# Performance work log

Hardware: AMD Instinct MI355X
Metric: run time of the kernel (lower is better)

## Reference

```python
import jax, jax.numpy as jnp
import numpy as np
import math

BS, S, D, H, DFF, L = 32, 512, 512, 8, 2048, 2
DK = D // H
K_INDEX = 5
NEG = -1e32


def _xavier(key, shape):
    fan_out, fan_in = shape[-2], shape[-1]
    lim = math.sqrt(6.0 / (fan_in + fan_out))
    return jax.random.uniform(key, shape, minval=-lim, maxval=lim, dtype=jnp.float32)


def _cosine_pe():
    pos = np.arange(S, dtype=np.float32)[:, None]
    div = np.exp(np.arange(0, D, 2, dtype=np.float32) * -(math.log(10000.0) / D))
    pe = np.zeros((S, D), dtype=np.float32)
    pe[:, 0::2] = np.sin(pos * div)
    pe[:, 1::2] = np.cos(pos * div)
    return jnp.asarray(pe)[None]  # [1,S,D]


def setup_inputs() -> dict:
    key = jax.random.key(0)
    ks = jax.random.split(key, 8)
    return {
        'q_embed_data': jax.random.normal(ks[0], (BS, S, D), jnp.float32),
        'qa_embed_data': jax.random.normal(ks[1], (BS, S, D), jnp.float32),
        'pe': _cosine_pe(),
        'Wk': _xavier(ks[2], (L, D, D)), 'bk': jnp.zeros((L, D)),
        'Wv': _xavier(ks[3], (L, D, D)), 'bv': jnp.zeros((L, D)),
        'Wo': _xavier(ks[4], (L, D, D)), 'bo': jnp.zeros((L, D)),
        'W1': _xavier(ks[5], (L, DFF, D)), 'b1': jnp.zeros((L, DFF)),
        'W2': _xavier(ks[6], (L, D, DFF)), 'b2': jnp.zeros((L, D)),
        'ln1w': jnp.ones((L, D)), 'ln1b': jnp.zeros((L, D)),
        'ln2w': jnp.ones((L, D)), 'ln2b': jnp.zeros((L, D)),
    }


def _ln(x, w, b):
    m = jnp.mean(x, axis=-1, keepdims=True)
    v = jnp.mean((x - m) ** 2, axis=-1, keepdims=True)
    return (x - m) / jnp.sqrt(v + 1e-5) * w + b


def _forward(q_embed_data, qa_embed_data, pe, Wk, bk, Wv, bv, Wo, bo,
             W1, b1, W2, b2, ln1w, ln1b, ln2w, ln2b):
    x = q_embed_data + pe[:, :S]
    y = qa_embed_data + pe[:, :S]
    # src_mask = (triu(ones, k=0) == 0): only strictly-lower positions allowed (row 0 fully masked)
    causal = jnp.tril(jnp.ones((S, S), bool), k=-1)
    attn_weights = None
    for l in range(L):
        # kq_same: q uses k_linear
        q = (x @ Wk[l].T + bk[l]).reshape(BS, S, H, DK).transpose(0, 2, 1, 3)
        k = q  # identical projection of identical input (key=query=x)
        v = (y @ Wv[l].T + bv[l]).reshape(BS, S, H, DK).transpose(0, 2, 1, 3)
        scores = jnp.einsum('bhqd,bhkd->bhqk', q, k) / math.sqrt(DK)
        scores = jnp.where(causal, scores, NEG)
        scores = jax.nn.softmax(scores, axis=-1)
        # sparseattn: for rows >= K_INDEX keep only entries >= k-th largest, re-softmax
        sb = scores[:, :, K_INDEX:, :]
        thr = jax.lax.top_k(sb, K_INDEX)[0][..., -1:]  # k-th largest per row
        sb = jnp.where(sb - thr >= 0, sb, NEG)
        scores = jnp.concatenate([scores[:, :, :K_INDEX, :], sb], axis=2)
        scores = jax.nn.softmax(scores, axis=-1)
        attn_weights = scores  # before_dropout_scores (before zero_pad)
        scores = scores.at[:, :, 0, :].set(0.0)  # zero_pad row 0
        out = jnp.einsum('bhqk,bhkd->bhqd', scores, v)
        out = out.transpose(0, 2, 1, 3).reshape(BS, S, D) @ Wo[l].T + bo[l]
        x = _ln(x + out, ln1w[l], ln1b[l])
        ff = jax.nn.relu(x @ W1[l].T + b1[l]) @ W2[l].T + b2[l]
        x = _ln(x + ff, ln2w[l], ln2b[l])
    return x, attn_weights


def reference(q_embed_data, qa_embed_data, pe, Wk, bk, Wv, bv, Wo, bo,
              W1, b1, W2, b2, ln1w, ln1b, ln2w, ln2b):
    return _forward(q_embed_data, qa_embed_data, pe, Wk, bk, Wv, bv, Wo, bo,
                    W1, b1, W2, b2, ln1w, ln1b, ln2w, ln2b)
```

## Files before the change

### kernel.cpp

```cpp
#include <hip/hip_runtime.h>
#include <hip/hip_bf16.h>
#include <math.h>

#define BSZ 32
#define SEQ 512
#define DIM 512
#define NH 8
#define DKH 64
#define DFFN 2048
#define NL 2
#define KIDX 5
#define NEGV -1e32f

typedef float f32x4 __attribute__((ext_vector_type(4)));
typedef short bf16x8 __attribute__((ext_vector_type(8)));
typedef unsigned short ushort_t;
typedef __attribute__((address_space(1))) void gvoid;
typedef __attribute__((address_space(3))) void lvoid;

__device__ __forceinline__ void gload_lds16(const void* g, void* l) {
    __builtin_amdgcn_global_load_lds((gvoid*)(uintptr_t)g, (lvoid*)l, 16, 0, 0);
}

__device__ __forceinline__ float wmaxf(float v) {
    #pragma unroll
    for (int m = 32; m > 0; m >>= 1) v = fmaxf(v, __shfl_xor(v, m));
    return v;
}
__device__ __forceinline__ float wsumf(float v) {
    #pragma unroll
    for (int m = 32; m > 0; m >>= 1) v += __shfl_xor(v, m);
    return v;
}
__device__ __forceinline__ int wsumi(int v) {
    #pragma unroll
    for (int m = 32; m > 0; m >>= 1) v += __shfl_xor(v, m);
    return v;
}

__device__ __forceinline__ unsigned int bf16_rne(float x) {
    unsigned int u = __float_as_uint(x);
    return (u + 0x7fffu + ((u >> 16) & 1u)) >> 16;
}
__device__ __forceinline__ void split3_8(const float* xs, unsigned int* hh,
                                         unsigned int* hm, unsigned int* hl) {
    #pragma unroll
    for (int e = 0; e < 8; e++) {
        float x = xs[e];
        unsigned int h0 = bf16_rne(x);
        float r1 = x - __uint_as_float(h0 << 16);
        unsigned int h1 = bf16_rne(r1);
        float r2 = r1 - __uint_as_float(h1 << 16);
        hh[e] = h0; hm[e] = h1; hl[e] = bf16_rne(r2);
    }
}
__device__ __forceinline__ uint4 pack8(const unsigned int* h) {
    return make_uint4(h[0] | (h[1] << 16), h[2] | (h[3] << 16),
                      h[4] | (h[5] << 16), h[6] | (h[7] << 16));
}

__device__ __forceinline__ f32x4 mfma_bf16(bf16x8 a, bf16x8 b, f32x4 c) {
    return __builtin_amdgcn_mfma_f32_16x16x32_bf16(a, b, c, 0, 0, 0);
}

__global__ void add_pe_old(const float4* __restrict__ q, const float4* __restrict__ qa,
                           const float4* __restrict__ pe, float4* __restrict__ x,
                           float4* __restrict__ y, int n4) {
    int i = blockIdx.x * 256 + threadIdx.x;
    if (i >= n4) return;
    int pi = i & (SEQ * DIM / 4 - 1);
    float4 p = pe[pi];
    float4 a = q[i], b = qa[i];
    x[i] = make_float4(a.x + p.x, a.y + p.y, a.z + p.z, a.w + p.w);
    y[i] = make_float4(b.x + p.x, b.y + p.y, b.z + p.z, b.w + p.w);
}

__global__ void add_pe_new(const float* __restrict__ q, const float* __restrict__ qa,
                           const float* __restrict__ pe, float* __restrict__ x,
                           ushort_t* __restrict__ ypl, size_t yelems, int n8) {
    int i = blockIdx.x * 256 + threadIdx.x;
    if (i >= n8) return;
    size_t base = (size_t)i * 8;
    size_t pb = base & (size_t)(SEQ * DIM - 1);
    float4 a0 = *(const float4*)(q + base), a1 = *(const float4*)(q + base + 4);
    float4 b0 = *(const float4*)(qa + base), b1 = *(const float4*)(qa + base + 4);
    float4 p0 = *(const float4*)(pe + pb), p1 = *(const float4*)(pe + pb + 4);
    float4 x0 = make_float4(a0.x + p0.x, a0.y + p0.y, a0.z + p0.z, a0.w + p0.w);
    float4 x1 = make_float4(a1.x + p1.x, a1.y + p1.y, a1.z + p1.z, a1.w + p1.w);
    *(float4*)(x + base) = x0;
    *(float4*)(x + base + 4) = x1;
    float ys[8] = {b0.x + p0.x, b0.y + p0.y, b0.z + p0.z, b0.w + p0.w,
                   b1.x + p1.x, b1.y + p1.y, b1.z + p1.z, b1.w + p1.w};
    unsigned int hh[8], hm[8], hl[8];
    split3_8(ys, hh, hm, hl);
    *(uint4*)(ypl + base) = pack8(hh);
    *(uint4*)(ypl + yelems + base) = pack8(hm);
    *(uint4*)(ypl + 2 * yelems + base) = pack8(hl);
}

__global__ void split3w(const float* __restrict__ W, ushort_t* __restrict__ out,
                        size_t elems, int n8) {
    int i = blockIdx.x * 256 + threadIdx.x;
    if (i >= n8) return;
    size_t base = (size_t)i * 8;
    float4 a0 = *(const float4*)(W + base), a1 = *(const float4*)(W + base + 4);
    float xs[8] = {a0.x, a0.y, a0.z, a0.w, a1.x, a1.y, a1.z, a1.w};
    unsigned int hh[8], hm[8], hl[8];
    split3_8(xs, hh, hm, hl);
    *(uint4*)(out + base) = pack8(hh);
    *(uint4*)(out + elems + base) = pack8(hm);
    *(uint4*)(out + 2 * elems + base) = pack8(hl);
}

template <int RELU>
__global__ __launch_bounds__(256)
void gemm_bt(const float* __restrict__ A, const float* __restrict__ B,
             const float* __restrict__ bias, float* __restrict__ C,
             int M, int N, int K) {
    __shared__ float As[16][132];
    __shared__ float Bs[16][132];
    const int tid = threadIdx.x;
    const int tx = tid & 15, ty = tid >> 4;
    const int m0 = blockIdx.y * 128, n0 = blockIdx.x * 128;
    float acc[8][8] = {};
    for (int k0 = 0; k0 < K; k0 += 16) {
        #pragma unroll
        for (int s = tid; s < 512; s += 256) {
            int r = s >> 2, c4 = s & 3;
            float4 va = *(const float4*)(A + (size_t)(m0 + r) * K + k0 + c4 * 4);
            As[c4 * 4 + 0][r] = va.x; As[c4 * 4 + 1][r] = va.y;
            As[c4 * 4 + 2][r] = va.z; As[c4 * 4 + 3][r] = va.w;
            float4 vb = *(const float4*)(B + (size_t)(n0 + r) * K + k0 + c4 * 4);
            Bs[c4 * 4 + 0][r] = vb.x; Bs[c4 * 4 + 1][r] = vb.y;
            Bs[c4 * 4 + 2][r] = vb.z; Bs[c4 * 4 + 3][r] = vb.w;
        }
        __syncthreads();
        #pragma unroll
        for (int kk = 0; kk < 16; kk++) {
            float a[8], b[8];
            *(float4*)&a[0] = *(const float4*)&As[kk][ty * 8];
            *(float4*)&a[4] = *(const float4*)&As[kk][ty * 8 + 4];
            *(float4*)&b[0] = *(const float4*)&Bs[kk][tx * 8];
            *(float4*)&b[4] = *(const float4*)&Bs[kk][tx * 8 + 4];
            #pragma unroll
            for (int i = 0; i < 8; i++)
                #pragma unroll
                for (int j = 0; j < 8; j++)
                    acc[i][j] = fmaf(a[i], b[j], acc[i][j]);
        }
        __syncthreads();
    }
    float bv[8];
    *(float4*)&bv[0] = *(const float4*)(bias + n0 + tx * 8);
    *(float4*)&bv[4] = *(const float4*)(bias + n0 + tx * 8 + 4);
    #pragma unroll
    for (int i = 0; i < 8; i++) {
        float out[8];
        #pragma unroll
        for (int j = 0; j < 8; j++) {
            float v = acc[i][j] + bv[j];
            if (RELU) v = fmaxf(v, 0.f);
            out[j] = v;
        }
        float* cp = C + (size_t)(m0 + ty * 8 + i) * N + n0 + tx * 8;
        *(float4*)cp = *(float4*)&out[0];
        *(float4*)(cp + 4) = *(float4*)&out[4];
    }
}

__global__ __launch_bounds__(256)
void scores128_kernel(const float* __restrict__ q, float* __restrict__ pbuf) {
    const int bh = blockIdx.y, b = bh >> 3, h = bh & 7;
    const int x = blockIdx.x;
    const int it = (x >= 6) ? 3 : (x >= 3) ? 2 : (x >= 1) ? 1 : 0;
    const int jt = x - it * (it + 1) / 2;
    const int m0 = it * 128, n0 = jt * 128;
    __shared__ float Qi[64][132];
    __shared__ float Qj[64][132];
    const float* qbase = q + (size_t)b * SEQ * DIM + h * DKH;
    const int tid = threadIdx.x;
    for (int s = tid; s < 2048; s += 256) {
        int row = (s & 15) | ((s >> 8) << 4);
        int c4 = (s >> 4) & 15;
        float4 vi = *(const float4*)(qbase + (size_t)(m0 + row) * DIM + c4 * 4);
        Qi[c4 * 4 + 0][row] = vi.x; Qi[c4 * 4 + 1][row] = vi.y;
        Qi[c4 * 4 + 2][row] = vi.z; Qi[c4 * 4 + 3][row] = vi.w;
        float4 vj = *(const float4*)(qbase + (size_t)(n0 + row) * DIM + c4 * 4);
        Qj[c4 * 4 + 0][row] = vj.x; Qj[c4 * 4 + 1][row] = vj.y;
        Qj[c4 * 4 + 2][row] = vj.z; Qj[c4 * 4 + 3][row] = vj.w;
    }
    __syncthreads();
    const int tx = tid & 15, ty = tid >> 4;
    float acc[8][8] = {};
    #pragma unroll 4
    for (int d = 0; d < 64; d++) {
        float a[8], bb[8];
        *(float4*)&a[0] = *(const float4*)&Qi[d][ty * 8];
        *(float4*)&a[4] = *(const float4*)&Qi[d][ty * 8 + 4];
        *(float4*)&bb[0] = *(const float4*)&Qj[d][tx * 8];
        *(float4*)&bb[4] = *(const float4*)&Qj[d][tx * 8 + 4];
        #pragma unroll
        for (int i = 0; i < 8; i++)
            #pragma unroll
            for (int j = 0; j < 8; j++)
                acc[i][j] = fmaf(a[i], bb[j], acc[i][j]);
    }
    float* prow = pbuf + ((size_t)bh * SEQ + m0) * SEQ + n0;
    #pragma unroll
    for (int i = 0; i < 8; i++) {
        int gi = m0 + ty * 8 + i;
        #pragma unroll
        for (int jq = 0; jq < 2; jq++) {
            float o[4];
            #pragma unroll
            for (int j = 0; j < 4; j++) {
                int gj = n0 + tx * 8 + jq * 4 + j;
                o[j] = (gj < gi) ? acc[i][jq * 4 + j] * 0.125f : NEGV;
            }
            *(float4*)(prow + (size_t)(ty * 8 + i) * SEQ + tx * 8 + jq * 4) = *(float4*)o;
        }
    }
}

template <int RELU, int OUTP, int NP>
__global__ __launch_bounds__(256) void gemm3p(
    const ushort_t* __restrict__ Apl, size_t Aelems, int lda,
    const ushort_t* __restrict__ Bpl, size_t Belems, int ldb,
    const float* __restrict__ bias,
    float* __restrict__ C, ushort_t* __restrict__ Cpl, size_t Celems,
    int ldc, int K) {
    constexpr int BB = NP * 512;
    __shared__ uint4 lds[2 * NP * 512];
    const int tid = threadIdx.x, lane = tid & 63, wid = tid >> 6;
    const int wm = wid >> 1, wn = wid & 1;
    const int m0 = blockIdx.y * 128, n0 = blockIdx.x * 128;
    const int lrow = lane & 15, lkof = (lane >> 4) * 8;
    f32x4 acc[4][4] = {};
    for (int k0 = 0; k0 < K; k0 += 32) {
        #pragma unroll
        for (int t = 0; t < 4 * NP; t++) {
            int cc = wid + t * 4;
            bool isB = cc >= 8 * NP;
            int c2 = isB ? (cc - 8 * NP) : cc;
            int p = c2 >> 3, fi = c2 & 7;
            const ushort_t* pb = isB ? (Bpl + (size_t)p * Belems) : (Apl + (size_t)p * Aelems);
            int ld = isB ? ldb : lda;
            int r0 = isB ? n0 : m0;
            const ushort_t* src = pb + (size_t)(r0 + fi * 16 + lrow) * ld + k0 + lkof;
            gload_lds16(src, &lds[(isB ? BB : 0) + p * 512 + fi * 64]);
        }
        __syncthreads();
        const bf16x8* ldsb = (const bf16x8*)lds;
        bf16x8 afr[4][NP];
        #pragma unroll
        for (int fm = 0; fm < 4; fm++)
            #pragma unroll
            for (int p = 0; p < NP; p++)
                afr[fm][p] = ldsb[p * 512 + (wm * 4 + fm) * 64 + lane];
        #pragma unroll
        for (int fn = 0; fn < 4; fn++) {
            bf16x8 b0 = ldsb[BB + 0 * 512 + (wn * 4 + fn) * 64 + lane];
            bf16x8 b1 = ldsb[BB + 1 * 512 + (wn * 4 + fn) * 64 + lane];
            bf16x8 b2;
            if constexpr (NP == 3) b2 = ldsb[BB + 2 * 512 + (wn * 4 + fn) * 64 + lane];
            #pragma unroll
            for (int fm = 0; fm < 4; fm++) {
                f32x4 t = acc[fm][fn];
                if constexpr (NP == 3) {
                    t = mfma_bf16(afr[fm][0], b0, t);
                    t = mfma_bf16(afr[fm][1], b0, t);
                    t = mfma_bf16(afr[fm][2], b0, t);
                    t = mfma_bf16(afr[fm][0], b1, t);
                    t = mfma_bf16(afr[fm][1], b1, t);
                    t = mfma_bf16(afr[fm][0], b2, t);
                } else {
                    t = mfma_bf16(afr[fm][0], b0, t);
                    t = mfma_bf16(afr[fm][1], b0, t);
                    t = mfma_bf16(afr[fm][0], b1, t);
                }
                acc[fm][fn] = t;
            }
        }
        __syncthreads();
    }
    #pragma unroll
    for (int fm = 0; fm < 4; fm++) {
        int row0 = m0 + (wm * 4 + fm) * 16 + (lane >> 4) * 4;
        #pragma unroll
        for (int fn = 0; fn < 4; fn++) {
            int col = n0 + (wn * 4 + fn) * 16 + (lane & 15);
            float bv = bias[col];
            f32x4 a = acc[fm][fn];
            #pragma unroll
            for (int r = 0; r < 4; r++) {
                int row = row0 + r;
                float val = a[r] + bv;
                if (RELU) val = fmaxf(val, 0.f);
                if constexpr (OUTP == 0) {
                    C[(size_t)row * ldc + col] = val;
                } else {
                    unsigned int h0 = bf16_rne(val);
                    float r1 = val - __uint_as_float(h0 << 16);
                    unsigned int h1 = bf16_rne(r1);
                    size_t o = (size_t)row * ldc + col;
                    Cpl[o] = (ushort_t)h0;
                    Cpl[Celems + o] = (ushort_t)h1;
                    if constexpr (NP == 3) {
                        float r2 = r1 - __uint_as_float(h1 << 16);
                        Cpl[2 * Celems + o] = (ushort_t)bf16_rne(r2);
                    }
                }
            }
        }
    }
}

template <int MODE, int TN>
__global__ __launch_bounds__(256) void mm6(const float* __restrict__ Aall,
                                           const float* __restrict__ Ball,
                                           float* __restrict__ Call,
                                           const float* __restrict__ bias,
                                           int lda, int ldb, int ldc, int K) {
    constexpr int BFR = TN / 16;
    constexpr int MFR = (TN == 128) ? 4 : 2;
    constexpr int BBASE = 3 * 8 * 64;
    __shared__ uint4 lds[3 * 8 * 64 + 3 * BFR * 64];

    const int tid = threadIdx.x, lane = tid & 63, wid = tid >> 6;
    const int wm = (TN == 128) ? (wid >> 1) : wid;
    const int wn = (TN == 128) ? (wid & 1) : 0;

    const float* A;
    const float* B;
    float* C;
    int m0, n0, kmax;
    if constexpr (MODE <= 1) {
        m0 = blockIdx.y * 128;
        n0 = blockIdx.x * 128;
        A = Aall; B = Ball; C = Call;
        kmax = K;
    } else {
        const int bh = blockIdx.y, b = bh >> 3, h = bh & 7, rb = blockIdx.x;
        m0 = rb * 128; n0 = 0;
        A = Aall + (size_t)bh * SEQ * SEQ;
        B = Ball + (size_t)bh * DKH * SEQ;
        C = Call + ((size_t)b * SEQ) * DIM + h * DKH;
        kmax = rb ? (rb + 1) * 128 : SEQ;
    }

    f32x4 acc[MFR][4] = {};

    for (int k0 = 0; k0 < kmax; k0 += 32) {
        for (int c = tid; c < (8 + BFR) * 64; c += 256) {
            int fi = c >> 6, lc = c & 63;
            const float* src = (fi < 8)
                ? A + (size_t)(m0 + fi * 16 + (lc & 15)) * lda + k0 + (lc >> 4) * 8
                : B + (size_t)(n0 + (fi - 8) * 16 + (lc & 15)) * ldb + k0 + (lc >> 4) * 8;
            float4 x0 = *(const float4*)src;
            float4 x1 = *(const float4*)(src + 4);
            float xs[8] = {x0.x, x0.y, x0.z, x0.w, x1.x, x1.y, x1.z, x1.w};
            unsigned int hh[8], hm[8], hl[8];
            split3_8(xs, hh, hm, hl);
            int base = (fi < 8) ? fi * 64 + lc : BBASE + (fi - 8) * 64 + lc;
            int fstride = (fi < 8) ? 8 * 64 : BFR * 64;
            lds[base + 0 * fstride] = pack8(hh);
            lds[base + 1 * fstride] = pack8(hm);
            lds[base + 2 * fstride] = pack8(hl);
        }
        __syncthreads();

        const bf16x8* ldsb = (const bf16x8*)lds;
        bf16x8 afr[MFR][3];
        #pragma unroll
        for (int fm = 0; fm < MFR; fm++)
            #pragma unroll
            for (int p = 0; p < 3; p++)
                afr[fm][p] = ldsb[p * 512 + (wm * MFR + fm) * 64 + lane];
        #pragma unroll
        for (int fn = 0; fn < 4; fn++) {
            bf16x8 b0 = ldsb[BBASE + 0 * (BFR * 64) + (wn * 4 + fn) * 64 + lane];
            bf16x8 b1 = ldsb[BBASE + 1 * (BFR * 64) + (wn * 4 + fn) * 64 + lane];
            bf16x8 b2 = ldsb[BBASE + 2 * (BFR * 64) + (wn * 4 + fn) * 64 + lane];
            #pragma unroll
            for (int fm = 0; fm < MFR; fm++) {
                f32x4 t = acc[fm][fn];
                t = mfma_bf16(afr[fm][0], b0, t);
                t = mfma_bf16(afr[fm][1], b0, t);
                t = mfma_bf16(afr[fm][2], b0, t);
                t = mfma_bf16(afr[fm][0], b1, t);
                t = mfma_bf16(afr[fm][1], b1, t);
                t = mfma_bf16(afr[fm][0], b2, t);
                acc[fm][fn] = t;
            }
        }
        __syncthreads();
    }

    #pragma unroll
    for (int fm = 0; fm < MFR; fm++) {
        int row0 = m0 + (wm * MFR + fm) * 16 + (lane >> 4) * 4;
        #pragma unroll
        for (int fn = 0; fn < 4; fn++) {
            int col = n0 + (wn * 4 + fn) * 16 + (lane & 15);
            float bv = 0.f;
            if constexpr (MODE <= 1) bv = bias[col];
            f32x4 a = acc[fm][fn];
            #pragma unroll
            for (int r = 0; r < 4; r++) {
                int row = row0 + r;
                float val;
                if constexpr (MODE == 0) val = a[r] + bv;
                else if constexpr (MODE == 1) val = fmaxf(a[r] + bv, 0.f);
                else val = (row == 0) ? 0.f : a[r];
                C[(size_t)row * ldc + col] = val;
            }
        }
    }
}

template <int NP>
__global__ __launch_bounds__(256) void mm6av_pl(const float* __restrict__ pbuf,
                                                const float* __restrict__ vt,
                                                ushort_t* __restrict__ Opl, size_t Oelems) {
    constexpr int BBASE = NP * 512;
    __shared__ uint4 lds[NP * 512 + NP * 256];
    const int tid = threadIdx.x, lane = tid & 63, wid = tid >> 6;
    const int bh = blockIdx.y, b = bh >> 3, h = bh & 7, rb = blockIdx.x;
    const int m0 = rb * 128;
    const float* A = pbuf + (size_t)bh * SEQ * SEQ;
    const float* B = vt + (size_t)bh * DKH * SEQ;
    const int kmax = rb ? (rb + 1) * 128 : SEQ;

    f32x4 acc[2][4] = {};
    for (int k0 = 0; k0 < kmax; k0 += 32) {
        for (int c = tid; c < 12 * 64; c += 256) {
            int fi = c >> 6, lc = c & 63;
            const float* src = (fi < 8)
                ? A + (size_t)(m0 + fi * 16 + (lc & 15)) * SEQ + k0 + (lc >> 4) * 8
                : B + (size_t)((fi - 8) * 16 + (lc & 15)) * SEQ + k0 + (lc >> 4) * 8;
            float4 x0 = *(const float4*)src;
            float4 x1 = *(const float4*)(src + 4);
            float xs[8] = {x0.x, x0.y, x0.z, x0.w, x1.x, x1.y, x1.z, x1.w};
            unsigned int hh[8], hm[8], hl[8];
            split3_8(xs, hh, hm, hl);
            int base, fstride;
            if (fi < 8) { base = fi * 64 + lc; fstride = 512; }
            else { base = BBASE + (fi - 8) * 64 + lc; fstride = 256; }
            lds[base] = pack8(hh);
            lds[base + fstride] = pack8(hm);
            if (NP == 3) lds[base + 2 * fstride] = pack8(hl);
        }
        __syncthreads();
        const bf16x8* ldsb = (const bf16x8*)lds;
        bf16x8 afr[2][NP];
        #pragma unroll
        for (int fm = 0; fm < 2; fm++)
            #pragma unroll
            for (int p = 0; p < NP; p++)
                afr[fm][p] = ldsb[p * 512 + (wid * 2 + fm) * 64 + lane];
        #pragma unroll
        for (int fn = 0; fn < 4; fn++) {
            bf16x8 b0 = ldsb[BBASE + 0 * 256 + fn * 64 + lane];
            bf16x8 b1 = ldsb[BBASE + 1 * 256 + fn * 64 + lane];
            bf16x8 b2;
            if constexpr (NP == 3) b2 = ldsb[BBASE + 2 * 256 + fn * 64 + lane];
            #pragma unroll
            for (int fm = 0; fm < 2; fm++) {
                f32x4 t = acc[fm][fn];
                if constexpr (NP == 3) {
                    t = mfma_bf16(afr[fm][0], b0, t);
                    t = mfma_bf16(afr[fm][1], b0, t);
                    t = mfma_bf16(afr[fm][2], b0, t);
                    t = mfma_bf16(afr[fm][0], b1, t);
                    t = mfma_bf16(afr[fm][1], b1, t);
                    t = mfma_bf16(afr[fm][0], b2, t);
                } else {
                    t = mfma_bf16(afr[fm][0], b0, t);
                    t = mfma_bf16(afr[fm][1], b0, t);
                    t = mfma_bf16(afr[fm][0], b1, t);
                }
                acc[fm][fn] = t;
            }
        }
        __syncthreads();
    }
    #pragma unroll
    for (int fm = 0; fm < 2; fm++) {
        int row0 = m0 + (wid * 2 + fm) * 16 + (lane >> 4) * 4;
        #pragma unroll
        for (int fn = 0; fn < 4; fn++) {
            int col = fn * 16 + (lane & 15);
            f32x4 a = acc[fm][fn];
            #pragma unroll
            for (int r = 0; r < 4; r++) {
                int row = row0 + r;
                float val = (row == 0) ? 0.f : a[r];
                unsigned int h0 = bf16_rne(val);
                float r1 = val - __uint_as_float(h0 << 16);
                unsigned int h1 = bf16_rne(r1);
                size_t o = ((size_t)b * SEQ + row) * DIM + h * DKH + col;
                Opl[o] = (ushort_t)h0;
                Opl[Oelems + o] = (ushort_t)h1;
                if constexpr (NP == 3) {
                    float r2 = r1 - __uint_as_float(h1 << 16);
                    Opl[2 * Oelems + o] = (ushort_t)bf16_rne(r2);
                }
            }
        }
    }
}

__global__ __launch_bounds__(256) void transpose_v_kernel(const float* __restrict__ v,
                                                          float* __restrict__ vt) {
    const int bh = blockIdx.y, jt = blockIdx.x;
    const int b = bh >> 3, h = bh & 7;
    __shared__ float L[64][65];
    const int tid = threadIdx.x;
    for (int s = tid; s < 1024; s += 256) {
        int jj = s >> 4, d4 = s & 15;
        float4 x = *(const float4*)(v + ((size_t)(b * SEQ) + jt * 64 + jj) * DIM + h * DKH + d4 * 4);
        L[jj][d4 * 4 + 0] = x.x; L[jj][d4 * 4 + 1] = x.y;
        L[jj][d4 * 4 + 2] = x.z; L[jj][d4 * 4 + 3] = x.w;
    }
    __syncthreads();
    int d = tid >> 2, jq = tid & 3;
    float* dst = vt + ((size_t)bh * DKH + d) * SEQ + jt * 64 + jq * 16;
    #pragma unroll
    for (int c4 = 0; c4 < 4; c4++) {
        float4 o = make_float4(L[jq * 16 + c4 * 4 + 0][d], L[jq * 16 + c4 * 4 + 1][d],
                               L[jq * 16 + c4 * 4 + 2][d], L[jq * 16 + c4 * 4 + 3][d]);
        *(float4*)(dst + c4 * 4) = o;
    }
}

__global__ __launch_bounds__(64)
void softmax_topk_kernel(float* __restrict__ pbuf) {
    const int i = blockIdx.x;
    const size_t row = (size_t)blockIdx.y * SEQ + i;
    const int lane = threadIdx.x;
    float* p = pbuf + row * SEQ;
    float v[8];
    {
        int j0 = lane * 4;
        if (j0 < i) {
            float4 x0 = *(const float4*)(p + j0);
            v[0] = (j0 + 0 < i) ? x0.x : NEGV;
            v[1] = (j0 + 1 < i) ? x0.y : NEGV;
            v[2] = (j0 + 2 < i) ? x0.z : NEGV;
            v[3] = (j0 + 3 < i) ? x0.w : NEGV;
        } else { v[0] = v[1] = v[2] = v[3] = NEGV; }
        int j1 = 256 + j0;
        if (j1 < i) {
            float4 x1 = *(const float4*)(p + j1);
            v[4] = (j1 + 0 < i) ? x1.x : NEGV;
            v[5] = (j1 + 1 < i) ? x1.y : NEGV;
            v[6] = (j1 + 2 < i) ? x1.z : NEGV;
            v[7] = (j1 + 3 < i) ? x1.w : NEGV;
        } else { v[4] = v[5] = v[6] = v[7] = NEGV; }
    }
    float lm = v[0];
    #pragma unroll
    for (int e = 1; e < 8; e++) lm = fmaxf(lm, v[e]);
    float m1 = wmaxf(lm);
    float ls = 0.f;
    #pragma unroll
    for (int e = 0; e < 8; e++) { v[e] = expf(v[e] - m1); ls += v[e]; }
    float Z = wsumf(ls);
    #pragma unroll
    for (int e = 0; e < 8; e++) v[e] = v[e] / Z;
    float thr = -INFINITY;
    if (i >= KIDX) {
        int remaining = KIDX;
        float cut = INFINITY;
        #pragma unroll 1
        for (int iter = 0; iter < KIDX; iter++) {
            float l2 = -INFINITY;
            #pragma unroll
            for (int e = 0; e < 8; e++) if (v[e] < cut) l2 = fmaxf(l2, v[e]);
            float m2 = wmaxf(l2);
            int lc = 0;
            #pragma unroll
            for (int e = 0; e < 8; e++) if (v[e] == m2) lc++;
            int c = wsumi(lc);
            if (c >= remaining) { thr = m2; break; }
            remaining -= c; cut = m2;
        }
    }
    float lpm = v[0];
    #pragma unroll
    for (int e = 1; e < 8; e++) lpm = fmaxf(lpm, v[e]);
    float pm = wmaxf(lpm);
    float t[8];
    float ls2 = 0.f;
    #pragma unroll
    for (int e = 0; e < 8; e++) {
        bool keep = (i >= KIDX) ? (v[e] >= thr) : true;
        t[e] = keep ? expf(v[e] - pm) : 0.f;
        ls2 += t[e];
    }
    float Z2 = wsumf(ls2);
    #pragma unroll
    for (int e = 0; e < 8; e++) t[e] = t[e] / Z2;
    *(float4*)(p + lane * 4) = make_float4(t[0], t[1], t[2], t[3]);
    *(float4*)(p + 256 + lane * 4) = make_float4(t[4], t[5], t[6], t[7]);
}

template <int EMIT>
__global__ __launch_bounds__(64)
void add_ln_kernel(const float* __restrict__ x, const float* __restrict__ t,
                   const float* __restrict__ w, const float* __restrict__ b,
                   float* __restrict__ dst, ushort_t* __restrict__ dpl, size_t delems) {
    const size_t row = blockIdx.x;
    const int lane = threadIdx.x;
    const float* xr = x + row * DIM;
    const float* tr = t + row * DIM;
    float v[8];
    {
        float4 a0 = *(const float4*)(xr + lane * 4);
        float4 t0 = *(const float4*)(tr + lane * 4);
        float4 a1 = *(const float4*)(xr + 256 + lane * 4);
        float4 t1 = *(const float4*)(tr + 256 + lane * 4);
        v[0] = a0.x + t0.x; v[1] = a0.y + t0.y; v[2] = a0.z + t0.z; v[3] = a0.w + t0.w;
        v[4] = a1.x + t1.x; v[5] = a1.y + t1.y; v[6] = a1.z + t1.z; v[7] = a1.w + t1.w;
    }
    float ls = 0.f;
    #pragma unroll
    for (int e = 0; e < 8; e++) ls += v[e];
    float mean = wsumf(ls) / (float)DIM;
    float ld = 0.f;
    #pragma unroll
    for (int e = 0; e < 8; e++) { float d = v[e] - mean; ld += d * d; }
    float var = wsumf(ld) / (float)DIM;
    float den = sqrtf(var + 1e-5f);
    float wv[8], bv[8];
    *(float4*)&wv[0] = *(const float4*)(w + lane * 4);
    *(float4*)&wv[4] = *(const float4*)(w + 256 + lane * 4);
    *(float4*)&bv[0] = *(const float4*)(b + lane * 4);
    *(float4*)&bv[4] = *(const float4*)(b + 256 + lane * 4);
    float o[8];
    #pragma unroll
    for (int e = 0; e < 8; e++) o[e] = (v[e] - mean) / den * wv[e] + bv[e];
    float* dr = dst + row * DIM;
    *(float4*)(dr + lane * 4) = make_float4(o[0], o[1], o[2], o[3]);
    *(float4*)(dr + 256 + lane * 4) = make_float4(o[4], o[5], o[6], o[7]);
    if constexpr (EMIT) {
        unsigned int hh[8], hm[8], hl[8];
        split3_8(o, hh, hm, hl);
        size_t base0 = row * DIM + lane * 4;
        size_t base1 = base0 + 256;
        #pragma unroll
        for (int p = 0; p < 3; p++) {
            const unsigned int* hp = (p == 0) ? hh : (p == 1) ? hm : hl;
            *(uint2*)(dpl + p * delems + base0) =
                make_uint2(hp[0] | (hp[1] << 16), hp[2] | (hp[3] << 16));
            *(uint2*)(dpl + p * delems + base1) =
                make_uint2(hp[4] | (hp[5] << 16), hp[6] | (hp[7] << 16));
        }
    }
}

extern "C" void kernel_launch(void* const* d_in, const int* in_sizes, int n_in,
                              void* d_out, int out_size, void* d_ws, size_t ws_size,
                              hipStream_t stream) {
    const float* q_embed = (const float*)d_in[0];
    const float* qa_embed = (const float*)d_in[1];
    const float* pe = (const float*)d_in[2];
    const float* Wk = (const float*)d_in[3];
    const float* bk = (const float*)d_in[4];
    const float* Wv = (const float*)d_in[5];
    const float* bv = (const float*)d_in[6];
    const float* Wo = (const float*)d_in[7];
    const float* bo = (const float*)d_in[8];
    const float* W1 = (const float*)d_in[9];
    const float* b1 = (const float*)d_in[10];
    const float* W2 = (const float*)d_in[11];
    const float* b2 = (const float*)d_in[12];
    const float* ln1w = (const float*)d_in[13];
    const float* ln1b = (const float*)d_in[14];
    const float* ln2w = (const float*)d_in[15];
    const float* ln2b = (const float*)d_in[16];

    float* outx = (float*)d_out;
    const size_t NE = (size_t)BSZ * SEQ * DIM;
    float* pbuf = outx + NE;
    float* ws = (float*)d_ws;
    const int M = BSZ * SEQ;

    const size_t need_new = 13 * NE * sizeof(float);
    if (ws_size >= need_new) {
        float* xbuf = ws;
        float* qbuf = ws + NE;
        float* vbuf = ws + 2 * NE;
        ushort_t* y_pl = (ushort_t*)(ws + 3 * NE);
        ushort_t* x_pl = (ushort_t*)(ws + 4 * NE + NE / 2);
        ushort_t* w_pl = (ushort_t*)(ws + 6 * NE);
        float* vt = ws + 7 * NE;
        ushort_t* o_pl = (ushort_t*)(ws + 8 * NE);
        ushort_t* h1_pl = (ushort_t*)(ws + 7 * NE);

        const size_t WVE = (size_t)DIM * DIM;
        const size_t W1E = (size_t)DFFN * DIM;
        const size_t LW = 3 * (WVE + WVE + W1E + W1E);

        for (int l = 0; l < NL; l++) {
            ushort_t* base = w_pl + (size_t)l * LW;
            split3w<<<(int)(WVE / 8 + 255) / 256, 256, 0, stream>>>(
                Wv + (size_t)l * WVE, base, WVE, (int)(WVE / 8));
            split3w<<<(int)(WVE / 8 + 255) / 256, 256, 0, stream>>>(
                Wo + (size_t)l * WVE, base + 3 * WVE, WVE, (int)(WVE / 8));
            split3w<<<(int)(W1E / 8 + 255) / 256, 256, 0, stream>>>(
                W1 + (size_t)l * W1E, base + 6 * WVE, W1E, (int)(W1E / 8));
            split3w<<<(int)(W1E / 8 + 255) / 256, 256, 0, stream>>>(
                W2 + (size_t)l * W1E, base + 6 * WVE + 3 * W1E, W1E, (int)(W1E / 8));
        }

        add_pe_new<<<(int)(NE / 8 + 255) / 256, 256, 0, stream>>>(
            q_embed, qa_embed, pe, xbuf, y_pl, NE, (int)(NE / 8));

        for (int l = 0; l < NL; l++) {
            ushort_t* wb = w_pl + (size_t)l * LW;
            ushort_t* Wv_pl = wb;
            ushort_t* Wo_pl = wb + 3 * WVE;
            ushort_t* W1_pl = wb + 6 * WVE;
            ushort_t* W2_pl = wb + 6 * WVE + 3 * W1E;

            gemm_bt<0><<<dim3(DIM / 128, M / 128), 256, 0, stream>>>(
                xbuf, Wk + (size_t)l * WVE, bk + (size_t)l * DIM, qbuf, M, DIM, DIM);
            if (l == 0) {
                gemm3p<0, 0, 3><<<dim3(DIM / 128, M / 128), 256, 0, stream>>>(
                    y_pl, NE, DIM, Wv_pl, WVE, DIM, bv + (size_t)l * DIM,
                    vbuf, nullptr, 0, DIM, DIM);
            } else {
                gemm3p<0, 0, 2><<<dim3(DIM / 128, M / 128), 256, 0, stream>>>(
                    y_pl, NE, DIM, Wv_pl, WVE, DIM, bv + (size_t)l * DIM,
                    vbuf, nullptr, 0, DIM, DIM);
            }
            transpose_v_kernel<<<dim3(8, BSZ * NH), 256, 0, stream>>>(vbuf, vt);
            scores128_kernel<<<dim3(10, BSZ * NH), 256, 0, stream>>>(qbuf, pbuf);
            softmax_topk_kernel<<<dim3(SEQ, BSZ * NH), 64, 0, stream>>>(pbuf);
            if (l == 0) {
                mm6av_pl<3><<<dim3(4, BSZ * NH), 256, 0, stream>>>(pbuf, vt, o_pl, NE);
                gemm3p<0, 0, 3><<<dim3(DIM / 128, M / 128), 256, 0, stream>>>(
                    o_pl, NE, DIM, Wo_pl, WVE, DIM, bo + (size_t)l * DIM,
                    qbuf, nullptr, 0, DIM, DIM);
            } else {
                mm6av_pl<2><<<dim3(4, BSZ * NH), 256, 0, stream>>>(pbuf, vt, o_pl, NE);
                gemm3p<0, 0, 2><<<dim3(DIM / 128, M / 128), 256, 0, stream>>>(
                    o_pl, NE, DIM, Wo_pl, WVE, DIM, bo + (size_t)l * DIM,
                    qbuf, nullptr, 0, DIM, DIM);
            }
            add_ln_kernel<1><<<M, 64, 0, stream>>>(
                xbuf, qbuf, ln1w + (size_t)l * DIM, ln1b + (size_t)l * DIM,
                xbuf, x_pl, NE);
            if (l == 0) {
                gemm3p<1, 1, 3><<<dim3(DFFN / 128, M / 128), 256, 0, stream>>>(
                    x_pl, NE, DIM, W1_pl, W1E, DIM, b1 + (size_t)l * DFFN,
                    nullptr, h1_pl, (size_t)M * DFFN, DFFN, DIM);
                gemm3p<0, 0, 3><<<dim3(DIM / 128, M / 128), 256, 0, stream>>>(
                    h1_pl, (size_t)M * DFFN, DFFN, W2_pl, W1E, DFFN, b2 + (size_t)l * DIM,
                    vbuf, nullptr, 0, DIM, DFFN);
            } else {
                gemm3p<1, 1, 2><<<dim3(DFFN / 128, M / 128), 256, 0, stream>>>(
                    x_pl, NE, DIM, W1_pl, W1E, DIM, b1 + (size_t)l * DFFN,
                    nullptr, h1_pl, (size_t)M * DFFN, DFFN, DIM);
                gemm3p<0, 0, 2><<<dim3(DIM / 128, M / 128), 256, 0, stream>>>(
                    h1_pl, (size_t)M * DFFN, DFFN, W2_pl, W1E, DFFN, b2 + (size_t)l * DIM,
                    vbuf, nullptr, 0, DIM, DFFN);
            }
            float* dst = (l == NL - 1) ? outx : xbuf;
            add_ln_kernel<0><<<M, 64, 0, stream>>>(
                xbuf, vbuf, ln2w + (size_t)l * DIM, ln2b + (size_t)l * DIM,
                dst, nullptr, 0);
        }
    } else {
        float* xbuf = ws;
        float* ybuf = ws + NE;
        float* qbuf = ws + 2 * NE;
        float* vbuf = ws + 3 * NE;
        float* obuf = ws + 4 * NE;
        float* vtbuf = ws + 5 * NE;
        float* h1buf = ws + 5 * NE;

        {
            int n4 = (int)(NE / 4);
            add_pe_old<<<(n4 + 255) / 256, 256, 0, stream>>>(
                (const float4*)q_embed, (const float4*)qa_embed, (const float4*)pe,
                (float4*)xbuf, (float4*)ybuf, n4);
        }
        for (int l = 0; l < NL; l++) {
            const float* Wk_l = Wk + (size_t)l * DIM * DIM;
            const float* Wv_l = Wv + (size_t)l * DIM * DIM;
            const float* Wo_l = Wo + (size_t)l * DIM * DIM;
            const float* W1_l = W1 + (size_t)l * DFFN * DIM;
            const float* W2_l = W2 + (size_t)l * DIM * DFFN;

            gemm_bt<0><<<dim3(DIM / 128, M / 128), 256, 0, stream>>>(
                xbuf, Wk_l, bk + (size_t)l * DIM, qbuf, M, DIM, DIM);
            mm6<0, 128><<<dim3(DIM / 128, M / 128), 256, 0, stream>>>(
                ybuf, Wv_l, vbuf, bv + (size_t)l * DIM, DIM, DIM, DIM, DIM);
            transpose_v_kernel<<<dim3(8, BSZ * NH), 256, 0, stream>>>(vbuf, vtbuf);
            scores128_kernel<<<dim3(10, BSZ * NH), 256, 0, stream>>>(qbuf, pbuf);
            softmax_topk_kernel<<<dim3(SEQ, BSZ * NH), 64, 0, stream>>>(pbuf);
            mm6<3, 64><<<dim3(4, BSZ * NH), 256, 0, stream>>>(
                pbuf, vtbuf, obuf, nullptr, SEQ, SEQ, DIM, SEQ);
            mm6<0, 128><<<dim3(DIM / 128, M / 128), 256, 0, stream>>>(
                obuf, Wo_l, qbuf, bo + (size_t)l * DIM, DIM, DIM, DIM, DIM);
            add_ln_kernel<0><<<M, 64, 0, stream>>>(
                xbuf, qbuf, ln1w + (size_t)l * DIM, ln1b + (size_t)l * DIM,
                xbuf, nullptr, 0);
            mm6<1, 128><<<dim3(DFFN / 128, M / 128), 256, 0, stream>>>(
                xbuf, W1_l, h1buf, b1 + (size_t)l * DFFN, DIM, DIM, DFFN, DIM);
            mm6<0, 128><<<dim3(DIM / 128, M / 128), 256, 0, stream>>>(
                h1buf, W2_l, vbuf, b2 + (size_t)l * DIM, DFFN, DFFN, DIM, DFFN);
            float* dst = (l == NL - 1) ? outx : xbuf;
            add_ln_kernel<0><<<M, 64, 0, stream>>>(
                xbuf, vbuf, ln2w + (size_t)l * DIM, ln2b + (size_t)l * DIM,
                dst, nullptr, 0);
        }
    }
}
```

Measured before the change: 1.970 ms.

## Replace dense attention-value GEMM with sparse top-k gather and XCD-aware GEMM tiling

The softmax/top-k kernel now emits a compact list of up to 16 nonzero weights and column indices per row, plus a count. A new per-row kernel gathers the matching V rows directly instead of running a dense split-precision MFMA over the full probability matrix. Rows with more survivors fall back to a dense dot over the full row. This removes the V transpose and most of the dense P·V work, at the cost of scattered V reads. Separately, gemm3p remaps block indices so that consecutive M tiles land on the same XCD, for better L2 reuse.

```diff
diff --git a/kernel.cpp b/kernel.cpp
--- a/kernel.cpp
+++ b/kernel.cpp
@@ -11,6 +11,7 @@
 #define NL 2
 #define KIDX 5
 #define NEGV -1e32f
+#define NROWS (BSZ * NH * SEQ)
 
 typedef float f32x4 __attribute__((ext_vector_type(4)));
 typedef short bf16x8 __attribute__((ext_vector_type(8)));
@@ -233,7 +234,13 @@
     __shared__ uint4 lds[2 * NP * 512];
     const int tid = threadIdx.x, lane = tid & 63, wid = tid >> 6;
     const int wm = wid >> 1, wn = wid & 1;
-    const int m0 = blockIdx.y * 128, n0 = blockIdx.x * 128;
+    const int nt = gridDim.x;
+    const int flat = blockIdx.y * nt + blockIdx.x;
+    const int xcd = flat & 7;
+    const int s_ = flat >> 3;
+    const int kk_ = s_ % nt;
+    const int pg = s_ / nt;
+    const int m0 = (pg * 8 + xcd) * 128, n0 = kk_ * 128;
     const int lrow = lane & 15, lkof = (lane >> 4) * 8;
     f32x4 acc[4][4] = {};
     for (int k0 = 0; k0 < K; k0 += 32) {
@@ -418,98 +425,6 @@
     }
 }
 
-template <int NP>
-__global__ __launch_bounds__(256) void mm6av_pl(const float* __restrict__ pbuf,
-                                                const float* __restrict__ vt,
-                                                ushort_t* __restrict__ Opl, size_t Oelems) {
-    constexpr int BBASE = NP * 512;
-    __shared__ uint4 lds[NP * 512 + NP * 256];
-    const int tid = threadIdx.x, lane = tid & 63, wid = tid >> 6;
-    const int bh = blockIdx.y, b = bh >> 3, h = bh & 7, rb = blockIdx.x;
-    const int m0 = rb * 128;
-    const float* A = pbuf + (size_t)bh * SEQ * SEQ;
-    const float* B = vt + (size_t)bh * DKH * SEQ;
-    const int kmax = rb ? (rb + 1) * 128 : SEQ;
-
-    f32x4 acc[2][4] = {};
-    for (int k0 = 0; k0 < kmax; k0 += 32) {
-        for (int c = tid; c < 12 * 64; c += 256) {
-            int fi = c >> 6, lc = c & 63;
-            const float* src = (fi < 8)
-                ? A + (size_t)(m0 + fi * 16 + (lc & 15)) * SEQ + k0 + (lc >> 4) * 8
-                : B + (size_t)((fi - 8) * 16 + (lc & 15)) * SEQ + k0 + (lc >> 4) * 8;
-            float4 x0 = *(const float4*)src;
-            float4 x1 = *(const float4*)(src + 4);
-            float xs[8] = {x0.x, x0.y, x0.z, x0.w, x1.x, x1.y, x1.z, x1.w};
-            unsigned int hh[8], hm[8], hl[8];
-            split3_8(xs, hh, hm, hl);
-            int base, fstride;
-            if (fi < 8) { base = fi * 64 + lc; fstride = 512; }
-            else { base = BBASE + (fi - 8) * 64 + lc; fstride = 256; }
-            lds[base] = pack8(hh);
-            lds[base + fstride] = pack8(hm);
-            if (NP == 3) lds[base + 2 * fstride] = pack8(hl);
-        }
-        __syncthreads();
-        const bf16x8* ldsb = (const bf16x8*)lds;
-        bf16x8 afr[2][NP];
-        #pragma unroll
-        for (int fm = 0; fm < 2; fm++)
-            #pragma unroll
-            for (int p = 0; p < NP; p++)
-                afr[fm][p] = ldsb[p * 512 + (wid * 2 + fm) * 64 + lane];
-        #pragma unroll
-        for (int fn = 0; fn < 4; fn++) {
-            bf16x8 b0 = ldsb[BBASE + 0 * 256 + fn * 64 + lane];
-            bf16x8 b1 = ldsb[BBASE + 1 * 256 + fn * 64 + lane];
-            bf16x8 b2;
-            if constexpr (NP == 3) b2 = ldsb[BBASE + 2 * 256 + fn * 64 + lane];
-            #pragma unroll
-            for (int fm = 0; fm < 2; fm++) {
-                f32x4 t = acc[fm][fn];
-                if constexpr (NP == 3) {
-                    t = mfma_bf16(afr[fm][0], b0, t);
-                    t = mfma_bf16(afr[fm][1], b0, t);
-                    t = mfma_bf16(afr[fm][2], b0, t);
-                    t = mfma_bf16(afr[fm][0], b1, t);
-                    t = mfma_bf16(afr[fm][1], b1, t);
-                    t = mfma_bf16(afr[fm][0], b2, t);
-                } else {
-                    t = mfma_bf16(afr[fm][0], b0, t);
-                    t = mfma_bf16(afr[fm][1], b0, t);
-                    t = mfma_bf16(afr[fm][0], b1, t);
-                }
-                acc[fm][fn] = t;
-            }
-        }
-        __syncthreads();
-    }
-    #pragma unroll
-    for (int fm = 0; fm < 2; fm++) {
-        int row0 = m0 + (wid * 2 + fm) * 16 + (lane >> 4) * 4;
-        #pragma unroll
-        for (int fn = 0; fn < 4; fn++) {
-            int col = fn * 16 + (lane & 15);
-            f32x4 a = acc[fm][fn];
-            #pragma unroll
-            for (int r = 0; r < 4; r++) {
-                int row = row0 + r;
-                float val = (row == 0) ? 0.f : a[r];
-                unsigned int h0 = bf16_rne(val);
-                float r1 = val - __uint_as_float(h0 << 16);
-                unsigned int h1 = bf16_rne(r1);
-                size_t o = ((size_t)b * SEQ + row) * DIM + h * DKH + col;
-                Opl[o] = (ushort_t)h0;
-                Opl[Oelems + o] = (ushort_t)h1;
-                if constexpr (NP == 3) {
-                    float r2 = r1 - __uint_as_float(h1 << 16);
-                    Opl[2 * Oelems + o] = (ushort_t)bf16_rne(r2);
-                }
-            }
-        }
-    }
-}
-
 __global__ __launch_bounds__(256) void transpose_v_kernel(const float* __restrict__ v,
                                                           float* __restrict__ vt) {
     const int bh = blockIdx.y, jt = blockIdx.x;
@@ -534,7 +449,8 @@
 }
 
 __global__ __launch_bounds__(64)
-void softmax_topk_kernel(float* __restrict__ pbuf) {
+void softmax_topk_kernel(float* __restrict__ pbuf, float* __restrict__ wl,
+                         unsigned int* __restrict__ il, int* __restrict__ cnt) {
     const int i = blockIdx.x;
     const size_t row = (size_t)blockIdx.y * SEQ + i;
     const int lane = threadIdx.x;
@@ -603,6 +519,72 @@
     for (int e = 0; e < 8; e++) t[e] = t[e] / Z2;
     *(float4*)(p + lane * 4) = make_float4(t[0], t[1], t[2], t[3]);
     *(float4*)(p + 256 + lane * 4) = make_float4(t[4], t[5], t[6], t[7]);
+    if (wl) {
+        int cv;
+        if (i == 0) cv = 0;
+        else if (i < KIDX) cv = 1000;
+        else {
+            unsigned long long mlt = (lane == 63) ? ~0ull >> 1 : ((1ull << (lane + 1)) - 1) >> 1;
+            mlt = ((1ull << lane)) - 1;
+            int base = 0;
+            #pragma unroll
+            for (int e = 0; e < 8; e++) {
+                bool k = (v[e] >= thr);
+                unsigned long long m = __ballot(k);
+                if (k) {
+                    int pos = base + (int)__popcll(m & mlt);
+                    if (pos < 16) {
+                        wl[row * 16 + pos] = t[e];
+                        il[row * 16 + pos] = (e < 4) ? (lane * 4 + e) : (256 + lane * 4 + e - 4);
+                    }
+                }
+                base += (int)__popcll(m);
+            }
+            cv = (base > 16) ? 1000 : base;
+        }
+        if (lane == 0) cnt[row] = cv;
+    }
+}
+
+template <int NP>
+__global__ __launch_bounds__(256) void av_fused(
+    const float* __restrict__ pbuf, const float* __restrict__ v,
+    const float* __restrict__ wl, const unsigned int* __restrict__ il,
+    const int* __restrict__ cnt, ushort_t* __restrict__ Opl, size_t Oelems) {
+    const int bh = blockIdx.y, b = bh >> 3, h = bh & 7;
+    const int wid = threadIdx.x >> 6, lane = threadIdx.x & 63;
+    const int i = blockIdx.x * 4 + wid;
+    const size_t row = (size_t)bh * SEQ + i;
+    const float* vb = v + ((size_t)b * SEQ) * DIM + h * DKH + lane;
+    float val = 0.f;
+    const int c = cnt[row];
+    if (c > 0 && c <= 16) {
+        for (int k = 0; k < c; k++) {
+            float w = wl[row * 16 + k];
+            unsigned int j = il[row * 16 + k];
+            val = fmaf(w, vb[(size_t)j * DIM], val);
+        }
+    } else if (c > 16) {
+        const float* pr = pbuf + row * SEQ;
+        float a0 = 0.f, a1 = 0.f, a2 = 0.f, a3 = 0.f;
+        for (int j = 0; j < SEQ; j += 4) {
+            a0 = fmaf(pr[j + 0], vb[(size_t)(j + 0) * DIM], a0);
+            a1 = fmaf(pr[j + 1], vb[(size_t)(j + 1) * DIM], a1);
+            a2 = fmaf(pr[j + 2], vb[(size_t)(j + 2) * DIM], a2);
+            a3 = fmaf(pr[j + 3], vb[(size_t)(j + 3) * DIM], a3);
+        }
+        val = (a0 + a1) + (a2 + a3);
+    }
+    unsigned int h0 = bf16_rne(val);
+    float r1 = val - __uint_as_float(h0 << 16);
+    unsigned int h1 = bf16_rne(r1);
+    size_t o = ((size_t)b * SEQ + i) * DIM + h * DKH + lane;
+    Opl[o] = (ushort_t)h0;
+    Opl[Oelems + o] = (ushort_t)h1;
+    if constexpr (NP == 3) {
+        float r2 = r1 - __uint_as_float(h1 << 16);
+        Opl[2 * Oelems + o] = (ushort_t)bf16_rne(r2);
+    }
 }
 
 template <int EMIT>
@@ -694,9 +676,11 @@
         ushort_t* y_pl = (ushort_t*)(ws + 3 * NE);
         ushort_t* x_pl = (ushort_t*)(ws + 4 * NE + NE / 2);
         ushort_t* w_pl = (ushort_t*)(ws + 6 * NE);
-        float* vt = ws + 7 * NE;
         ushort_t* o_pl = (ushort_t*)(ws + 8 * NE);
         ushort_t* h1_pl = (ushort_t*)(ws + 7 * NE);
+        float* wl = qbuf;
+        unsigned int* il = (unsigned int*)(qbuf + 16 * (size_t)NROWS);
+        int* cntp = (int*)(qbuf + 32 * (size_t)NROWS);
 
         const size_t WVE = (size_t)DIM * DIM;
         const size_t W1E = (size_t)DFFN * DIM;
@@ -735,16 +719,17 @@
                     y_pl, NE, DIM, Wv_pl, WVE, DIM, bv + (size_t)l * DIM,
                     vbuf, nullptr, 0, DIM, DIM);
             }
-            transpose_v_kernel<<<dim3(8, BSZ * NH), 256, 0, stream>>>(vbuf, vt);
             scores128_kernel<<<dim3(10, BSZ * NH), 256, 0, stream>>>(qbuf, pbuf);
-            softmax_topk_kernel<<<dim3(SEQ, BSZ * NH), 64, 0, stream>>>(pbuf);
+            softmax_topk_kernel<<<dim3(SEQ, BSZ * NH), 64, 0, stream>>>(pbuf, wl, il, cntp);
             if (l == 0) {
-                mm6av_pl<3><<<dim3(4, BSZ * NH), 256, 0, stream>>>(pbuf, vt, o_pl, NE);
+                av_fused<3><<<dim3(SEQ / 4, BSZ * NH), 256, 0, stream>>>(
+                    pbuf, vbuf, wl, il, cntp, o_pl, NE);
                 gemm3p<0, 0, 3><<<dim3(DIM / 128, M / 128), 256, 0, stream>>>(
                     o_pl, NE, DIM, Wo_pl, WVE, DIM, bo + (size_t)l * DIM,
                     qbuf, nullptr, 0, DIM, DIM);
             } else {
-                mm6av_pl<2><<<dim3(4, BSZ * NH), 256, 0, stream>>>(pbuf, vt, o_pl, NE);
+                av_fused<2><<<dim3(SEQ / 4, BSZ * NH), 256, 0, stream>>>(
+                    pbuf, vbuf, wl, il, cntp, o_pl, NE);
                 gemm3p<0, 0, 2><<<dim3(DIM / 128, M / 128), 256, 0, stream>>>(
                     o_pl, NE, DIM, Wo_pl, WVE, DIM, bo + (size_t)l * DIM,
                     qbuf, nullptr, 0, DIM, DIM);
@@ -800,7 +785,8 @@
                 ybuf, Wv_l, vbuf, bv + (size_t)l * DIM, DIM, DIM, DIM, DIM);
             transpose_v_kernel<<<dim3(8, BSZ * NH), 256, 0, stream>>>(vbuf, vtbuf);
             scores128_kernel<<<dim3(10, BSZ * NH), 256, 0, stream>>>(qbuf, pbuf);
-            softmax_topk_kernel<<<dim3(SEQ, BSZ * NH), 64, 0, stream>>>(pbuf);
+            softmax_topk_kernel<<<dim3(SEQ, BSZ * NH), 64, 0, stream>>>(
+                pbuf, nullptr, nullptr, nullptr);
             mm6<3, 64><<<dim3(4, BSZ * NH), 256, 0, stream>>>(
                 pbuf, vtbuf, obuf, nullptr, SEQ, SEQ, DIM, SEQ);
             mm6<0, 128><<<dim3(DIM / 128, M / 128), 256, 0, stream>>>(
```

Result: slower. 2.165 ms (+9.9%).
